# Kernel tuning notes

Measured on AMD Instinct MI355X. Metric: run time of the kernel, lower is better.

Reference implementation:

```python
import jax, jax.numpy as jnp
import numpy as np

EMBED_DIM = 1024
NUM_HEADS = 16
HEAD_DIM = EMBED_DIM // NUM_HEADS
SCALE = HEAD_DIM ** -0.5


def setup_inputs() -> dict:
    key = jax.random.key(0)
    ks = jax.random.split(key, 9)
    B, N = 2, 2048
    s = EMBED_DIM ** -0.5  # ~ torch Linear init scale
    x = jax.random.normal(ks[0], (B, N, EMBED_DIM), dtype=jnp.float32)
    Wq = jax.random.uniform(ks[1], (EMBED_DIM, EMBED_DIM), jnp.float32, -s, s)
    bq = jax.random.uniform(ks[2], (EMBED_DIM,), jnp.float32, -s, s)
    Wk = jax.random.uniform(ks[3], (EMBED_DIM, EMBED_DIM), jnp.float32, -s, s)
    bk = jax.random.uniform(ks[4], (EMBED_DIM,), jnp.float32, -s, s)
    Wv = jax.random.uniform(ks[5], (EMBED_DIM, EMBED_DIM), jnp.float32, -s, s)
    bv = jax.random.uniform(ks[6], (EMBED_DIM,), jnp.float32, -s, s)
    Wo = jax.random.uniform(ks[7], (EMBED_DIM, EMBED_DIM), jnp.float32, -s, s)
    bo = jax.random.uniform(ks[8], (EMBED_DIM,), jnp.float32, -s, s)
    return {"x": x, "Wq": Wq, "bq": bq, "Wk": Wk, "bk": bk,
            "Wv": Wv, "bv": bv, "Wo": Wo, "bo": bo}


def reference(x, Wq, bq, Wk, bk, Wv, bv, Wo, bo):
    B, N, R = x.shape
    H, D = NUM_HEADS, HEAD_DIM
    # projections: Linear(x) = x @ W^T + b; reshape to (B, H, N, D)
    def proj(W, b):
        return (x @ W.T + b).reshape(B, N, H, D).transpose(0, 2, 1, 3)
    q = proj(Wq, bq)
    k = proj(Wk, bk)
    v = proj(Wv, bv)
    attn = jnp.einsum('bhnd,bhmd->bhnm', q, k) * SCALE  # (B,H,N,N)
    attn = jax.nn.softmax(attn, axis=-1)
    out = jnp.einsum('bhnm,bhmd->bhnd', attn, v)        # (B,H,N,D)
    out = out.transpose(0, 2, 1, 3).reshape(B, N, R)
    return out @ Wo.T + bo
```

## Files before the change

### kernel.cpp

```cpp
#include <hip/hip_runtime.h>
#include <stdint.h>

typedef __bf16 bf16;
typedef __bf16 bf16x2 __attribute__((ext_vector_type(2)));
typedef __bf16 bf16x4 __attribute__((ext_vector_type(4)));
typedef __bf16 bf16x8 __attribute__((ext_vector_type(8)));
typedef float f32x4 __attribute__((ext_vector_type(4)));
typedef short short4_t __attribute__((ext_vector_type(4)));

#define MFMA16(a, b, c) __builtin_amdgcn_mfma_f32_16x16x32_bf16((a), (b), (c), 0, 0, 0)

__device__ __forceinline__ f32x4 mfma1k(bf16x4 a, bf16x4 b, f32x4 c) {
    return __builtin_amdgcn_mfma_f32_16x16x16bf16_1k(
        __builtin_bit_cast(short4_t, a), __builtin_bit_cast(short4_t, b), c, 0, 0, 0);
}

#define EMBED 1024
#define SEQ   2048
#define MROWS 4096
#define HDIM  64
#define ATTN_SCALE 0.125f

__device__ __forceinline__ void gl2lds16(const bf16* g, bf16* l) {
    __builtin_amdgcn_global_load_lds(
        (const __attribute__((address_space(1))) void*)g,
        (__attribute__((address_space(3))) void*)l,
        16, 0, 0);
}

__global__ __launch_bounds__(256) void cast_all_kernel(
    const float* __restrict__ x,  const float* __restrict__ Wq,
    const float* __restrict__ Wk, const float* __restrict__ Wv,
    const float* __restrict__ Wo, bf16* __restrict__ dst) {
    const int blk = blockIdx.x;
    const float* src;
    size_t so, dofs;
    if (blk < 2048) {
        src = x; so = (size_t)blk * 2048; dofs = so;
    } else {
        const int w = (blk - 2048) >> 9;
        so  = (size_t)((blk - 2048) & 511) * 2048;
        src = (w == 0) ? Wq : (w == 1) ? Wk : (w == 2) ? Wv : Wo;
        dofs = (size_t)(4 + w) * 1024 * 1024 + so;
    }
    const size_t i = (size_t)threadIdx.x * 8;
    float4 a = *(const float4*)(src + so + i);
    float4 b = *(const float4*)(src + so + i + 4);
    bf16x8 o;
    o[0] = (bf16)a.x; o[1] = (bf16)a.y; o[2] = (bf16)a.z; o[3] = (bf16)a.w;
    o[4] = (bf16)b.x; o[5] = (bf16)b.y; o[6] = (bf16)b.z; o[7] = (bf16)b.w;
    *(bf16x8*)(dst + dofs + i) = o;
}

template <typename OutT>
__device__ __forceinline__ void gemm_tile(const bf16* __restrict__ A,
                                          const bf16* __restrict__ W,
                                          const float* __restrict__ bias,
                                          OutT* __restrict__ C,
                                          int m0, int n0) {
    __shared__ bf16 As[128 * 64];
    __shared__ bf16 Bs[128 * 64];

    const int lane = threadIdx.x & 63;
    const int wv   = threadIdx.x >> 6;
    const int wm   = (wv >> 1) * 64;
    const int wn   = (wv & 1) * 64;
    const int fr   = lane & 15;
    const int quad = lane >> 4;
    const int srow = wv * 8 + (lane >> 3);
    const int swz  = (((lane & 7) ^ ((lane >> 3) & 7))) * 8;

    f32x4 acc[4][4];
#pragma unroll
    for (int mt = 0; mt < 4; ++mt)
#pragma unroll
        for (int nt = 0; nt < 4; ++nt)
            acc[mt][nt] = (f32x4){0.f, 0.f, 0.f, 0.f};

    for (int k0 = 0; k0 < 1024; k0 += 64) {
#pragma unroll
        for (int i = 0; i < 4; ++i) {
            gl2lds16(A + (size_t)(m0 + i * 32 + srow) * 1024 + k0 + swz,
                     &As[(i * 32 + wv * 8) * 64]);
            gl2lds16(W + (size_t)(n0 + i * 32 + srow) * 1024 + k0 + swz,
                     &Bs[(i * 32 + wv * 8) * 64]);
        }
        __syncthreads();
#pragma unroll
        for (int ks = 0; ks < 2; ++ks) {
            const int fcol = ((ks * 4 + quad) ^ (fr & 7)) * 8;
            bf16x8 af[4], bfr[4];
#pragma unroll
            for (int t = 0; t < 4; ++t) {
                af[t]  = *(const bf16x8*)&As[(wm + t * 16 + fr) * 64 + fcol];
                bfr[t] = *(const bf16x8*)&Bs[(wn + t * 16 + fr) * 64 + fcol];
            }
#pragma unroll
            for (int mt = 0; mt < 4; ++mt)
#pragma unroll
                for (int nt = 0; nt < 4; ++nt)
                    acc[mt][nt] = MFMA16(af[mt], bfr[nt], acc[mt][nt]);
        }
        __syncthreads();
    }

    float bv[4];
#pragma unroll
    for (int nt = 0; nt < 4; ++nt)
        bv[nt] = bias[n0 + wn + nt * 16 + fr];
    const int row4 = quad * 4;
#pragma unroll
    for (int mt = 0; mt < 4; ++mt)
#pragma unroll
        for (int nt = 0; nt < 4; ++nt)
#pragma unroll
            for (int r = 0; r < 4; ++r) {
                int m = m0 + wm + mt * 16 + row4 + r;
                int n = n0 + wn + nt * 16 + fr;
                C[(size_t)m * 1024 + n] = (OutT)(acc[mt][nt][r] + bv[nt]);
            }
}

__global__ __launch_bounds__(256) void qkv_kernel(
    const bf16* __restrict__ x,
    const bf16* __restrict__ Wq, const float* __restrict__ bq,
    const bf16* __restrict__ Wk, const float* __restrict__ bk,
    const bf16* __restrict__ Wv, const float* __restrict__ bv,
    bf16* __restrict__ Q, bf16* __restrict__ K, bf16* __restrict__ V) {
    const int m0    = blockIdx.x * 128;
    const int which = blockIdx.y >> 3;
    const int n0    = (blockIdx.y & 7) * 128;
    const bf16*  W = (which == 0) ? Wq : (which == 1) ? Wk : Wv;
    const float* b = (which == 0) ? bq : (which == 1) ? bk : bv;
    bf16*        C = (which == 0) ? Q  : (which == 1) ? K  : V;
    gemm_tile<bf16>(x, W, b, C, m0, n0);
}

__global__ __launch_bounds__(256) void oproj_kernel(
    const bf16* __restrict__ O, const bf16* __restrict__ Wo,
    const float* __restrict__ bo, float* __restrict__ out) {
    gemm_tile<float>(O, Wo, bo, out, blockIdx.x * 128, blockIdx.y * 128);
}

__global__ __launch_bounds__(256) void attn_kernel(
    const bf16* __restrict__ Q, const bf16* __restrict__ K,
    const bf16* __restrict__ V, bf16* __restrict__ O) {
    const int lane = threadIdx.x & 63;
    const int wv   = threadIdx.x >> 6;
    const int quad = lane >> 4;
    const int f    = lane & 15;
    const int q0   = blockIdx.x * 64;
    const int b    = blockIdx.y >> 4;
    const int h    = blockIdx.y & 15;

    const size_t base = ((size_t)b * SEQ) * 1024 + (size_t)h * 64;
    const bf16* Qp = Q + base;
    const bf16* Kp = K + base;
    const bf16* Vp = V + base;
    bf16*       Op = O + base;

    __shared__ bf16 Ks[2][64 * 64];
    __shared__ bf16 VTs[2][64 * 72];

    bf16x8 qf[2];
    {
        const bf16* qrow = Qp + (size_t)(q0 + wv * 16 + f) * 1024;
        qf[0] = *(const bf16x8*)(qrow + quad * 8);
        qf[1] = *(const bf16x8*)(qrow + 32 + quad * 8);
    }

    const int srow = wv * 8 + (lane >> 3);
    const int swz  = (((lane & 7) ^ ((lane >> 3) & 7))) * 8;
    auto stageK = [&](int kv0, int buf) {
#pragma unroll
        for (int i = 0; i < 2; ++i)
            gl2lds16(Kp + (size_t)(kv0 + i * 32 + srow) * 1024 + swz,
                     &Ks[buf][(i * 32 + wv * 8) * 64]);
    };
    const int vkv = (lane & 31) * 2;
    const int vd0 = wv * 16 + (lane >> 5) * 8;
    auto loadVa = [&](int kv0) {
        return *(const bf16x8*)(Vp + (size_t)(kv0 + vkv) * 1024 + vd0);
    };
    auto loadVb = [&](int kv0) {
        return *(const bf16x8*)(Vp + (size_t)(kv0 + vkv + 1) * 1024 + vd0);
    };
    auto writeV = [&](bf16x8 va, bf16x8 vb, int buf) {
#pragma unroll
        for (int j = 0; j < 8; ++j) {
            bf16x2 pr = {va[j], vb[j]};
            *(bf16x2*)&VTs[buf][(vd0 + j) * 72 + vkv] = pr;
        }
    };

    stageK(0, 0);
    {
        bf16x8 va = loadVa(0), vb = loadVb(0);
        writeV(va, vb, 0);
    }

    f32x4 oacc[4];
#pragma unroll
    for (int t = 0; t < 4; ++t)
        oacc[t] = (f32x4){0.f, 0.f, 0.f, 0.f};
    float l_part = 0.f;

    __syncthreads();

    for (int it = 0; it < SEQ / 64; ++it) {
        const int cur = it & 1;
        bf16x8 nva, nvb;
        const bool more = (it + 1 < SEQ / 64);
        if (more) {
            nva = loadVa((it + 1) * 64);
            nvb = loadVb((it + 1) * 64);
            stageK((it + 1) * 64, 1 - cur);
        }

        f32x4 s[4];
#pragma unroll
        for (int t = 0; t < 4; ++t)
            s[t] = (f32x4){0.f, 0.f, 0.f, 0.f};
#pragma unroll
        for (int ks = 0; ks < 2; ++ks) {
            const int fcol = ((ks * 4 + quad) ^ (f & 7)) * 8;
            bf16x8 kf[4];
#pragma unroll
            for (int t = 0; t < 4; ++t)
                kf[t] = *(const bf16x8*)&Ks[cur][(t * 16 + f) * 64 + fcol];
#pragma unroll
            for (int t = 0; t < 4; ++t)
                s[t] = MFMA16(kf[t], qf[ks], s[t]);
        }

        bf16x4 pb[4];
#pragma unroll
        for (int t = 0; t < 4; ++t)
#pragma unroll
            for (int r = 0; r < 4; ++r) {
                float p = __expf(s[t][r] * ATTN_SCALE);
                l_part += p;
                pb[t][r] = (bf16)p;
            }

#pragma unroll
        for (int dt = 0; dt < 4; ++dt) {
#pragma unroll
            for (int kt = 0; kt < 4; ++kt) {
                bf16x4 vf = *(const bf16x4*)&VTs[cur][(dt * 16 + f) * 72 + kt * 16 + quad * 4];
                oacc[dt] = mfma1k(vf, pb[kt], oacc[dt]);
            }
        }

        if (more)
            writeV(nva, nvb, 1 - cur);
        __syncthreads();
    }

    l_part += __shfl_xor(l_part, 16);
    l_part += __shfl_xor(l_part, 32);
    const float inv = 1.0f / l_part;

    bf16* orow = Op + (size_t)(q0 + wv * 16 + f) * 1024;
#pragma unroll
    for (int dt = 0; dt < 4; ++dt) {
        bf16x4 ov;
#pragma unroll
        for (int r = 0; r < 4; ++r)
            ov[r] = (bf16)(oacc[dt][r] * inv);
        *(bf16x4*)(orow + dt * 16 + quad * 4) = ov;
    }
}

extern "C" void kernel_launch(void* const* d_in, const int* in_sizes, int n_in,
                              void* d_out, int out_size, void* d_ws, size_t ws_size,
                              hipStream_t stream) {
    const float* x  = (const float*)d_in[0];
    const float* Wq = (const float*)d_in[1];
    const float* bq = (const float*)d_in[2];
    const float* Wk = (const float*)d_in[3];
    const float* bk = (const float*)d_in[4];
    const float* Wv = (const float*)d_in[5];
    const float* bv = (const float*)d_in[6];
    const float* Wo = (const float*)d_in[7];
    const float* bo = (const float*)d_in[8];
    float* out = (float*)d_out;

    bf16* xb  = (bf16*)d_ws;
    bf16* Wqb = xb  + (size_t)MROWS * 1024;
    bf16* Wkb = Wqb + (size_t)1024 * 1024;
    bf16* Wvb = Wkb + (size_t)1024 * 1024;
    bf16* Wob = Wvb + (size_t)1024 * 1024;
    bf16* Q   = Wob + (size_t)1024 * 1024;
    bf16* K   = Q + (size_t)MROWS * 1024;
    bf16* V   = K + (size_t)MROWS * 1024;
    bf16* O   = V + (size_t)MROWS * 1024;

    cast_all_kernel<<<4096, 256, 0, stream>>>(x, Wq, Wk, Wv, Wo, xb);

    qkv_kernel<<<dim3(32, 24), 256, 0, stream>>>(xb, Wqb, bq, Wkb, bk, Wvb, bv, Q, K, V);
    attn_kernel<<<dim3(32, 32), 256, 0, stream>>>(Q, K, V, O);
    oproj_kernel<<<dim3(32, 8), 256, 0, stream>>>(O, Wob, bo, out);
}
```

Before: 211.3 us.

## Write V transposed from QKV GEMM, stage via async LDS loads; split oproj tiles

The QKV projection now writes V in a transposed (B*H*D, N) layout. The attention kernel can then stage V^T tiles with direct global-to-LDS loads and an XOR swizzle, replacing register loads followed by a scattered transpose-write into padded shared memory. This moves the transpose cost out of the attention inner loop and frees registers and VALU work there, at the price of strided 8-byte stores in the GEMM epilogue. The output projection also switches to 128x64 tiles, doubling its grid from 256 to 512 blocks for better CU occupancy on the small GEMM.

```diff
diff --git a/kernel.cpp b/kernel.cpp
--- a/kernel.cpp
+++ b/kernel.cpp
@@ -18,7 +18,6 @@
 #define EMBED 1024
 #define SEQ   2048
 #define MROWS 4096
-#define HDIM  64
 #define ATTN_SCALE 0.125f
 
 __device__ __forceinline__ void gl2lds16(const bf16* g, bf16* l) {
@@ -52,7 +51,7 @@
     *(bf16x8*)(dst + dofs + i) = o;
 }
 
-template <typename OutT>
+template <typename OutT, bool V_TRANS>
 __device__ __forceinline__ void gemm_tile(const bf16* __restrict__ A,
                                           const bf16* __restrict__ W,
                                           const float* __restrict__ bias,
@@ -112,13 +111,25 @@
 #pragma unroll
     for (int mt = 0; mt < 4; ++mt)
 #pragma unroll
-        for (int nt = 0; nt < 4; ++nt)
-#pragma unroll
-            for (int r = 0; r < 4; ++r) {
-                int m = m0 + wm + mt * 16 + row4 + r;
-                int n = n0 + wn + nt * 16 + fr;
-                C[(size_t)m * 1024 + n] = (OutT)(acc[mt][nt][r] + bv[nt]);
-            }
+        for (int nt = 0; nt < 4; ++nt) {
+            if (V_TRANS) {
+                const int m  = m0 + wm + mt * 16 + row4;
+                const int n  = n0 + wn + nt * 16 + fr;
+                const int bb = m >> 11, t = m & 2047;
+                bf16x4 ov;
+#pragma unroll
+                for (int r = 0; r < 4; ++r)
+                    ov[r] = (bf16)(acc[mt][nt][r] + bv[nt]);
+                *(bf16x4*)&C[((size_t)(bb * 1024 + n)) * 2048 + t] = ov;
+            } else {
+#pragma unroll
+                for (int r = 0; r < 4; ++r) {
+                    int m = m0 + wm + mt * 16 + row4 + r;
+                    int n = n0 + wn + nt * 16 + fr;
+                    C[(size_t)m * 1024 + n] = (OutT)(acc[mt][nt][r] + bv[nt]);
+                }
+            }
+        }
 }
 
 __global__ __launch_bounds__(256) void qkv_kernel(
@@ -126,25 +137,94 @@
     const bf16* __restrict__ Wq, const float* __restrict__ bq,
     const bf16* __restrict__ Wk, const float* __restrict__ bk,
     const bf16* __restrict__ Wv, const float* __restrict__ bv,
-    bf16* __restrict__ Q, bf16* __restrict__ K, bf16* __restrict__ V) {
+    bf16* __restrict__ Q, bf16* __restrict__ K, bf16* __restrict__ VT) {
     const int m0    = blockIdx.x * 128;
     const int which = blockIdx.y >> 3;
     const int n0    = (blockIdx.y & 7) * 128;
-    const bf16*  W = (which == 0) ? Wq : (which == 1) ? Wk : Wv;
-    const float* b = (which == 0) ? bq : (which == 1) ? bk : bv;
-    bf16*        C = (which == 0) ? Q  : (which == 1) ? K  : V;
-    gemm_tile<bf16>(x, W, b, C, m0, n0);
+    if (which == 2) {
+        gemm_tile<bf16, true>(x, Wv, bv, VT, m0, n0);
+    } else {
+        const bf16*  W = (which == 0) ? Wq : Wk;
+        const float* b = (which == 0) ? bq : bk;
+        bf16*        C = (which == 0) ? Q  : K;
+        gemm_tile<bf16, false>(x, W, b, C, m0, n0);
+    }
 }
 
 __global__ __launch_bounds__(256) void oproj_kernel(
-    const bf16* __restrict__ O, const bf16* __restrict__ Wo,
-    const float* __restrict__ bo, float* __restrict__ out) {
-    gemm_tile<float>(O, Wo, bo, out, blockIdx.x * 128, blockIdx.y * 128);
+    const bf16* __restrict__ A, const bf16* __restrict__ W,
+    const float* __restrict__ bias, float* __restrict__ C) {
+    const int m0 = blockIdx.x * 128;
+    const int n0 = blockIdx.y * 64;
+
+    __shared__ bf16 As[128 * 64];
+    __shared__ bf16 Bs[64 * 64];
+
+    const int lane = threadIdx.x & 63;
+    const int wv   = threadIdx.x >> 6;
+    const int wm   = (wv >> 1) * 64;
+    const int wn   = (wv & 1) * 32;
+    const int fr   = lane & 15;
+    const int quad = lane >> 4;
+    const int srow = wv * 8 + (lane >> 3);
+    const int swz  = (((lane & 7) ^ ((lane >> 3) & 7))) * 8;
+
+    f32x4 acc[4][2];
+#pragma unroll
+    for (int mt = 0; mt < 4; ++mt)
+#pragma unroll
+        for (int nt = 0; nt < 2; ++nt)
+            acc[mt][nt] = (f32x4){0.f, 0.f, 0.f, 0.f};
+
+    for (int k0 = 0; k0 < 1024; k0 += 64) {
+#pragma unroll
+        for (int i = 0; i < 4; ++i)
+            gl2lds16(A + (size_t)(m0 + i * 32 + srow) * 1024 + k0 + swz,
+                     &As[(i * 32 + wv * 8) * 64]);
+#pragma unroll
+        for (int i = 0; i < 2; ++i)
+            gl2lds16(W + (size_t)(n0 + i * 32 + srow) * 1024 + k0 + swz,
+                     &Bs[(i * 32 + wv * 8) * 64]);
+        __syncthreads();
+#pragma unroll
+        for (int ks = 0; ks < 2; ++ks) {
+            const int fcol = ((ks * 4 + quad) ^ (fr & 7)) * 8;
+            bf16x8 af[4], bfr[2];
+#pragma unroll
+            for (int t = 0; t < 4; ++t)
+                af[t] = *(const bf16x8*)&As[(wm + t * 16 + fr) * 64 + fcol];
+#pragma unroll
+            for (int t = 0; t < 2; ++t)
+                bfr[t] = *(const bf16x8*)&Bs[(wn + t * 16 + fr) * 64 + fcol];
+#pragma unroll
+            for (int mt = 0; mt < 4; ++mt)
+#pragma unroll
+                for (int nt = 0; nt < 2; ++nt)
+                    acc[mt][nt] = MFMA16(af[mt], bfr[nt], acc[mt][nt]);
+        }
+        __syncthreads();
+    }
+
+    float bv[2];
+#pragma unroll
+    for (int nt = 0; nt < 2; ++nt)
+        bv[nt] = bias[n0 + wn + nt * 16 + fr];
+    const int row4 = quad * 4;
+#pragma unroll
+    for (int mt = 0; mt < 4; ++mt)
+#pragma unroll
+        for (int nt = 0; nt < 2; ++nt)
+#pragma unroll
+            for (int r = 0; r < 4; ++r) {
+                int m = m0 + wm + mt * 16 + row4 + r;
+                int n = n0 + wn + nt * 16 + fr;
+                C[(size_t)m * 1024 + n] = acc[mt][nt][r] + bv[nt];
+            }
 }
 
 __global__ __launch_bounds__(256) void attn_kernel(
     const bf16* __restrict__ Q, const bf16* __restrict__ K,
-    const bf16* __restrict__ V, bf16* __restrict__ O) {
+    const bf16* __restrict__ VT, bf16* __restrict__ O) {
     const int lane = threadIdx.x & 63;
     const int wv   = threadIdx.x >> 6;
     const int quad = lane >> 4;
@@ -153,14 +233,13 @@
     const int b    = blockIdx.y >> 4;
     const int h    = blockIdx.y & 15;
 
-    const size_t base = ((size_t)b * SEQ) * 1024 + (size_t)h * 64;
-    const bf16* Qp = Q + base;
-    const bf16* Kp = K + base;
-    const bf16* Vp = V + base;
-    bf16*       Op = O + base;
+    const bf16* Qp = Q + ((size_t)b * SEQ) * 1024 + (size_t)h * 64;
+    const bf16* Kp = K + ((size_t)b * SEQ) * 1024 + (size_t)h * 64;
+    const bf16* Vp = VT + ((size_t)(b * 1024 + h * 64)) * 2048;
+    bf16*       Op = O + ((size_t)b * SEQ) * 1024 + (size_t)h * 64;
 
     __shared__ bf16 Ks[2][64 * 64];
-    __shared__ bf16 VTs[2][64 * 72];
+    __shared__ bf16 VTs[2][64 * 64];
 
     bf16x8 qf[2];
     {
@@ -177,27 +256,15 @@
             gl2lds16(Kp + (size_t)(kv0 + i * 32 + srow) * 1024 + swz,
                      &Ks[buf][(i * 32 + wv * 8) * 64]);
     };
-    const int vkv = (lane & 31) * 2;
-    const int vd0 = wv * 16 + (lane >> 5) * 8;
-    auto loadVa = [&](int kv0) {
-        return *(const bf16x8*)(Vp + (size_t)(kv0 + vkv) * 1024 + vd0);
+    auto stageVT = [&](int kv0, int buf) {
+#pragma unroll
+        for (int i = 0; i < 2; ++i)
+            gl2lds16(Vp + (size_t)(i * 32 + srow) * 2048 + kv0 + swz,
+                     &VTs[buf][(i * 32 + wv * 8) * 64]);
     };
-    auto loadVb = [&](int kv0) {
-        return *(const bf16x8*)(Vp + (size_t)(kv0 + vkv + 1) * 1024 + vd0);
-    };
-    auto writeV = [&](bf16x8 va, bf16x8 vb, int buf) {
-#pragma unroll
-        for (int j = 0; j < 8; ++j) {
-            bf16x2 pr = {va[j], vb[j]};
-            *(bf16x2*)&VTs[buf][(vd0 + j) * 72 + vkv] = pr;
-        }
-    };
 
     stageK(0, 0);
-    {
-        bf16x8 va = loadVa(0), vb = loadVb(0);
-        writeV(va, vb, 0);
-    }
+    stageVT(0, 0);
 
     f32x4 oacc[4];
 #pragma unroll
@@ -209,12 +276,9 @@
 
     for (int it = 0; it < SEQ / 64; ++it) {
         const int cur = it & 1;
-        bf16x8 nva, nvb;
-        const bool more = (it + 1 < SEQ / 64);
-        if (more) {
-            nva = loadVa((it + 1) * 64);
-            nvb = loadVb((it + 1) * 64);
+        if (it + 1 < SEQ / 64) {
             stageK((it + 1) * 64, 1 - cur);
+            stageVT((it + 1) * 64, 1 - cur);
         }
 
         f32x4 s[4];
@@ -247,13 +311,12 @@
         for (int dt = 0; dt < 4; ++dt) {
 #pragma unroll
             for (int kt = 0; kt < 4; ++kt) {
-                bf16x4 vf = *(const bf16x4*)&VTs[cur][(dt * 16 + f) * 72 + kt * 16 + quad * 4];
+                const int pc = ((kt * 2 + (quad >> 1)) ^ (f & 7)) * 8 + (quad & 1) * 4;
+                bf16x4 vf = *(const bf16x4*)&VTs[cur][(dt * 16 + f) * 64 + pc];
                 oacc[dt] = mfma1k(vf, pb[kt], oacc[dt]);
             }
         }
 
-        if (more)
-            writeV(nva, nvb, 1 - cur);
         __syncthreads();
     }
 
@@ -293,12 +356,12 @@
     bf16* Wob = Wvb + (size_t)1024 * 1024;
     bf16* Q   = Wob + (size_t)1024 * 1024;
     bf16* K   = Q + (size_t)MROWS * 1024;
-    bf16* V   = K + (size_t)MROWS * 1024;
-    bf16* O   = V + (size_t)MROWS * 1024;
+    bf16* VT  = K + (size_t)MROWS * 1024;
+    bf16* O   = VT + (size_t)MROWS * 1024;
 
     cast_all_kernel<<<4096, 256, 0, stream>>>(x, Wq, Wk, Wv, Wo, xb);
 
-    qkv_kernel<<<dim3(32, 24), 256, 0, stream>>>(xb, Wqb, bq, Wkb, bk, Wvb, bv, Q, K, V);
-    attn_kernel<<<dim3(32, 32), 256, 0, stream>>>(Q, K, V, O);
-    oproj_kernel<<<dim3(32, 8), 256, 0, stream>>>(O, Wob, bo, out);
-}
+    qkv_kernel<<<dim3(32, 24), 256, 0, stream>>>(xb, Wqb, bq, Wkb, bk, Wvb, bv, Q, K, VT);
+    attn_kernel<<<dim3(32, 32), 256, 0, stream>>>(Q, K, VT, O);
+    oproj_kernel<<<dim3(32, 16), 256, 0, stream>>>(O, Wob, bo, out);
+}
```

After: 212.9 us. About the same (+0.8%).
